# Kernel optimization log

Measured on AMD Instinct MI355X. Metric: run time of the kernel, lower is better.

The kernel has to match this reference:

```python
import jax, jax.numpy as jnp
import numpy as np
from jax import lax


def _box_conv3d(x, win):
    k = jnp.ones((1, 1, win, win, win), x.dtype) / float(win ** 3)
    pad = win // 2
    return lax.conv_general_dilated(
        x, k,
        window_strides=(1, 1, 1),
        padding=[(pad, pad)] * 3,
        dimension_numbers=('NCDHW', 'OIDHW', 'NCDHW'),
    )


def setup_inputs() -> dict:
    key = jax.random.key(0)
    k1, k2 = jax.random.split(key)
    shape = (1, 1, 160, 192, 224)
    pred = jax.random.uniform(k1, shape, dtype=jnp.float32)
    target = jax.random.uniform(k2, shape, dtype=jnp.float32)
    return {'pred': pred, 'target': target, 'window_size': 9}


def reference(pred, target, window_size):
    Ii = target
    Ji = pred
    win = window_size
    mu1 = _box_conv3d(Ii, win)
    mu2 = _box_conv3d(Ji, win)
    mu1_sq = mu1 * mu1
    mu2_sq = mu2 * mu2
    mu1_mu2 = mu1 * mu2
    sigma1_sq = _box_conv3d(Ii * Ii, win) - mu1_sq
    sigma2_sq = _box_conv3d(Ji * Ji, win) - mu2_sq
    sigma12 = _box_conv3d(Ii * Ji, win) - mu1_mu2
    eps = jnp.finfo(sigma12.dtype).eps
    cc = sigma12 * sigma12 / jnp.maximum(sigma1_sq * sigma2_sq, eps)
    return -jnp.mean(cc)
```

## Files before the change

kernel.cpp:

```cpp
#include <hip/hip_runtime.h>
#include <hip/hip_fp16.h>

#define D_  160
#define H_  192
#define W_  224
#define HW_ (H_ * W_)
#define HW2_ (HW_ / 2)
#define N_  (D_ * H_ * W_)
#define INV729 (1.0f / 729.0f)
#define HSEG 16
#define NSEG (H_ / HSEG)
#define NROW (HSEG + 9)
#define UPD  (NSEG * 2)


__device__ __forceinline__ unsigned pack2(float a, float b) {
    const __half2 h = __floats2half2_rn(a, b);
    return *(const unsigned*)&h;
}

__global__ __launch_bounds__(64) void k_passWH(const float* __restrict__ pred,
                                               const float* __restrict__ targ,
                                               uint4* __restrict__ outA,
                                               unsigned* __restrict__ outB,
                                               double* __restrict__ acc) {
    __shared__ __attribute__((aligned(16))) float2 lds[2][128];
    if (blockIdx.x == 0 && threadIdx.x == 0) *acc = 0.0;

    const int lane = threadIdx.x;
    const int unit = blockIdx.x;
    const int d    = unit / UPD;
    const int rem  = unit % UPD;
    const int half = rem & 1;
    const int h0   = (rem >> 1) * HSEG;
    const long dbase = (long)d * HW_;
    const int wbase = half * 112;

    const bool isld = (lane < 30);
    const int  w0c  = wbase - 4 + 4 * lane;
    const bool cok  = isld && (w0c >= 0) && (w0c + 3 < W_);
    const int  wsc  = w0c < 0 ? 0 : (w0c > W_ - 4 ? W_ - 4 : w0c);
    const float* gI = targ + dbase + wsc;
    const float* gJ = pred + dbase + wsc;

    float2 q[5][9];
    #pragma unroll
    for (int c = 0; c < 5; ++c)
        #pragma unroll
        for (int k = 0; k < 9; ++k) q[c][k] = make_float2(0.f, 0.f);
    float S0[5] = {0,0,0,0,0}, S1[5] = {0,0,0,0,0};

    float4 pI[3], pJ[3];
    auto fetch = [&](int r, float4& fi, float4& fj) {
        if (r >= NROW) { fi = make_float4(0.f,0.f,0.f,0.f); fj = fi; return; }
        const int hh = h0 - 5 + r;
        const int hc = hh < 0 ? 0 : (hh >= H_ ? H_ - 1 : hh);
        float4 a = *(const float4*)(gI + (long)hc * W_);
        float4 b = *(const float4*)(gJ + (long)hc * W_);
        if (!(cok && hh >= 0 && hh < H_)) {
            a = make_float4(0.f, 0.f, 0.f, 0.f); b = a;
        }
        fi = a; fj = b;
    };
    auto wr = [&](int row, int slot) {
        float2* dst = &lds[row & 1][4 * lane];
        *(float4*)(dst)     = make_float4(pI[slot].x, pJ[slot].x, pI[slot].y, pJ[slot].y);
        *(float4*)(dst + 2) = make_float4(pI[slot].z, pJ[slot].z, pI[slot].w, pJ[slot].w);
    };

    if (isld) {
        fetch(0, pI[0], pJ[0]);
        fetch(1, pI[1], pJ[1]);
        fetch(2, pI[2], pJ[2]);
        wr(0, 0);
        fetch(3, pI[0], pJ[0]);
    }

    #pragma unroll
    for (int p = 0; p < NROW; ++p) {
        if (isld) {
            wr(p + 1, (p + 1) % 3);
            fetch(p + 4, pI[(p + 1) % 3], pJ[(p + 1) % 3]);
        }

        if (lane < 56) {
            float x[10], y[10];
            #pragma unroll
            for (int m = 0; m < 5; ++m) {
                const float4 v = *(const float4*)&lds[p & 1][2 * lane + 2 * m];
                x[2*m] = v.x; y[2*m] = v.y; x[2*m+1] = v.z; y[2*m+1] = v.w;
            }
            float sI = 0.f, sJ = 0.f, sII = 0.f, sJJ = 0.f, sIJ = 0.f;
            #pragma unroll
            for (int kk = 0; kk < 9; ++kk) {
                sI  += x[kk];          sJ  += y[kk];
                sII = fmaf(x[kk], x[kk], sII);
                sJJ = fmaf(y[kk], y[kk], sJJ);
                sIJ = fmaf(x[kk], y[kk], sIJ);
            }
            float w0[5], w1[5];
            w0[0] = sI;  w1[0] = sI  + x[9] - x[0];
            w0[1] = sJ;  w1[1] = sJ  + y[9] - y[0];
            w0[2] = sII; w1[2] = sII + x[9]*x[9] - x[0]*x[0];
            w0[3] = sJJ; w1[3] = sJJ + y[9]*y[9] - y[0]*y[0];
            w0[4] = sIJ; w1[4] = sIJ + x[9]*y[9] - x[0]*y[0];

            const int ph = p % 9;
            #pragma unroll
            for (int c = 0; c < 5; ++c) {
                S0[c] += w0[c] - q[c][ph].x;
                S1[c] += w1[c] - q[c][ph].y;
                q[c][ph].x = w0[c];
                q[c][ph].y = w1[c];
            }
            if (p >= 9) {
                const long rb = dbase + (long)(h0 + p - 9) * W_;
                uint4 oA;
                oA.x = pack2(S0[0], S0[1]); oA.y = pack2(S0[2], S0[3]);
                oA.z = pack2(S1[0], S1[1]); oA.w = pack2(S1[2], S1[3]);
                outA[rb / 2 + half * 56 + lane] = oA;
                outB[rb / 2 + half * 56 + lane] = pack2(S0[4], S1[4]);
            }
        }
    }
}

__global__ __launch_bounds__(256) void k_passD(const uint4* __restrict__ bufA,
                                               const unsigned* __restrict__ bufB,
                                               double* __restrict__ acc) {
    const int DSEG = D_ / 8;
    const int p2 = blockIdx.x * blockDim.x + threadIdx.x;
    const int d0 = blockIdx.y * DSEG;

    float2 q[5][9], S[5];
    #pragma unroll
    for (int c = 0; c < 5; ++c) S[c] = make_float2(0.f, 0.f);

    #pragma unroll
    for (int k = 0; k < 9; ++k) {
        const int dd = d0 - 5 + k;
        uint4 va = make_uint4(0u, 0u, 0u, 0u);
        unsigned vb = 0u;
        if (dd >= 0) {
            va = bufA[(long)dd * HW2_ + p2];
            vb = bufB[(long)dd * HW2_ + p2];
        }
        const float2 a01 = __half22float2(*(const __half2*)&va.x);
        const float2 a23 = __half22float2(*(const __half2*)&va.y);
        const float2 b01 = __half22float2(*(const __half2*)&va.z);
        const float2 b23 = __half22float2(*(const __half2*)&va.w);
        const float2 c44 = __half22float2(*(const __half2*)&vb);
        q[0][k] = make_float2(a01.x, b01.x); S[0].x += a01.x; S[0].y += b01.x;
        q[1][k] = make_float2(a01.y, b01.y); S[1].x += a01.y; S[1].y += b01.y;
        q[2][k] = make_float2(a23.x, b23.x); S[2].x += a23.x; S[2].y += b23.x;
        q[3][k] = make_float2(a23.y, b23.y); S[3].x += a23.y; S[3].y += b23.y;
        q[4][k] = make_float2(c44.x, c44.y); S[4].x += c44.x; S[4].y += c44.y;
    }

    float myacc = 0.f;
    #pragma unroll
    for (int j = 0; j < DSEG; ++j) {
        const int dd = d0 + 4 + j;
        uint4 va = make_uint4(0u, 0u, 0u, 0u);
        unsigned vb = 0u;
        if (dd < D_) {
            va = bufA[(long)dd * HW2_ + p2];
            vb = bufB[(long)dd * HW2_ + p2];
        }
        const float2 a01 = __half22float2(*(const __half2*)&va.x);
        const float2 a23 = __half22float2(*(const __half2*)&va.y);
        const float2 b01 = __half22float2(*(const __half2*)&va.z);
        const float2 b23 = __half22float2(*(const __half2*)&va.w);
        const float2 c44 = __half22float2(*(const __half2*)&vb);
        const float2 nv[5] = {
            make_float2(a01.x, b01.x), make_float2(a01.y, b01.y),
            make_float2(a23.x, b23.x), make_float2(a23.y, b23.y),
            make_float2(c44.x, c44.y)
        };
        const int ph = j % 9;
        #pragma unroll
        for (int c = 0; c < 5; ++c) {
            S[c].x += nv[c].x - q[c][ph].x;
            S[c].y += nv[c].y - q[c][ph].y;
            q[c][ph] = nv[c];
        }
        #pragma unroll
        for (int e = 0; e < 2; ++e) {
            const float mu1 = (e ? S[0].y : S[0].x) * INV729;
            const float mu2 = (e ? S[1].y : S[1].x) * INV729;
            const float s1  = (e ? S[2].y : S[2].x) * INV729 - mu1 * mu1;
            const float s2  = (e ? S[3].y : S[3].x) * INV729 - mu2 * mu2;
            const float s12 = (e ? S[4].y : S[4].x) * INV729 - mu1 * mu2;
            const float den = fmaxf(s1 * s2, 1.1920929e-7f);
            myacc += (s12 * s12) / den;
        }
    }

    __shared__ float red[256];
    red[threadIdx.x] = myacc;
    __syncthreads();
    #pragma unroll
    for (int s = 128; s > 0; s >>= 1) {
        if (threadIdx.x < s) red[threadIdx.x] += red[threadIdx.x + s];
        __syncthreads();
    }
    if (threadIdx.x == 0) atomicAdd(acc, (double)red[0]);
}

__global__ void k_fin(const double* __restrict__ acc, float* __restrict__ out) {
    out[0] = (float)(-(*acc) / (double)N_);
}

extern "C" void kernel_launch(void* const* d_in, const int* in_sizes, int n_in,
                              void* d_out, int out_size, void* d_ws, size_t ws_size,
                              hipStream_t stream) {
    const float* pred = (const float*)d_in[0];
    const float* targ = (const float*)d_in[1];

    uint4*    bufA = (uint4*)d_ws;
    unsigned* bufB = (unsigned*)((char*)d_ws + (size_t)(N_ / 2) * 16);
    double*   acc  = (double*)((char*)d_ws + (size_t)(N_ / 2) * 16 + (size_t)(N_ / 2) * 4);
    float*    out  = (float*)d_out;

    k_passWH<<<D_ * UPD, 64, 0, stream>>>(pred, targ, bufA, bufB, acc);
    dim3 g3(HW2_ / 256, 8);
    k_passD<<<g3, 256, 0, stream>>>(bufA, bufB, acc);
    k_fin<<<1, 1, 0, stream>>>(acc, out);
}
```

Baseline: 58.37 us.

## Process two depth slices per WH block and store H-ring history as packed half

Each 64-lane block of the W/H box-sum pass now handles two depth slices (d and d+80), using 60 lanes for loads instead of 30 and running the per-row column-sum work twice. The launch grid is halved accordingly. To fit two slices' ring buffers in registers, the 9-entry H-direction history is stored as packed fp16 pairs, and the running sums subtract the rounded value that was actually stored. This raises load-lane utilisation and per-thread work, at the cost of more registers, fewer blocks, and extra half conversions.

```diff
diff --git a/kernel.cpp b/kernel.cpp
--- a/kernel.cpp
+++ b/kernel.cpp
@@ -24,31 +24,37 @@
                                                uint4* __restrict__ outA,
                                                unsigned* __restrict__ outB,
                                                double* __restrict__ acc) {
-    __shared__ __attribute__((aligned(16))) float2 lds[2][128];
+    __shared__ __attribute__((aligned(16))) float2 lds[2][2][128];
     if (blockIdx.x == 0 && threadIdx.x == 0) *acc = 0.0;
 
     const int lane = threadIdx.x;
     const int unit = blockIdx.x;
-    const int d    = unit / UPD;
+    const int dp   = unit / UPD;
     const int rem  = unit % UPD;
     const int half = rem & 1;
     const int h0   = (rem >> 1) * HSEG;
-    const long dbase = (long)d * HW_;
+    const long dbaseA = (long)dp * HW_;
+    const long dbaseB = (long)(dp + 80) * HW_;
     const int wbase = half * 112;
 
-    const bool isld = (lane < 30);
-    const int  w0c  = wbase - 4 + 4 * lane;
-    const bool cok  = isld && (w0c >= 0) && (w0c + 3 < W_);
+    const int  sj   = (lane < 30) ? lane : lane - 30;
+    const int  w0c  = wbase - 4 + 4 * sj;
+    const bool cokG = (lane < 60) && (w0c >= 0) && (w0c + 3 < W_);
     const int  wsc  = w0c < 0 ? 0 : (w0c > W_ - 4 ? W_ - 4 : w0c);
-    const float* gI = targ + dbase + wsc;
-    const float* gJ = pred + dbase + wsc;
-
-    float2 q[5][9];
-    #pragma unroll
-    for (int c = 0; c < 5; ++c)
+    const long sdb  = (lane < 30) ? dbaseA : dbaseB;
+    const int  sstr = (lane < 30) ? 0 : 1;
+    const float* gI = targ + sdb + wsc;
+    const float* gJ = pred + sdb + wsc;
+
+    unsigned q[2][5][9];
+    #pragma unroll
+    for (int s = 0; s < 2; ++s)
         #pragma unroll
-        for (int k = 0; k < 9; ++k) q[c][k] = make_float2(0.f, 0.f);
-    float S0[5] = {0,0,0,0,0}, S1[5] = {0,0,0,0,0};
+        for (int c = 0; c < 5; ++c)
+            #pragma unroll
+            for (int k = 0; k < 9; ++k) q[s][c][k] = 0u;
+    float S0[2][5] = {{0,0,0,0,0},{0,0,0,0,0}};
+    float S1[2][5] = {{0,0,0,0,0},{0,0,0,0,0}};
 
     float4 pI[3], pJ[3];
     auto fetch = [&](int r, float4& fi, float4& fj) {
@@ -57,18 +63,18 @@
         const int hc = hh < 0 ? 0 : (hh >= H_ ? H_ - 1 : hh);
         float4 a = *(const float4*)(gI + (long)hc * W_);
         float4 b = *(const float4*)(gJ + (long)hc * W_);
-        if (!(cok && hh >= 0 && hh < H_)) {
+        if (!(cokG && hh >= 0 && hh < H_)) {
             a = make_float4(0.f, 0.f, 0.f, 0.f); b = a;
         }
         fi = a; fj = b;
     };
     auto wr = [&](int row, int slot) {
-        float2* dst = &lds[row & 1][4 * lane];
+        float2* dst = &lds[sstr][row & 1][4 * sj];
         *(float4*)(dst)     = make_float4(pI[slot].x, pJ[slot].x, pI[slot].y, pJ[slot].y);
         *(float4*)(dst + 2) = make_float4(pI[slot].z, pJ[slot].z, pI[slot].w, pJ[slot].w);
     };
 
-    if (isld) {
+    if (lane < 60) {
         fetch(0, pI[0], pJ[0]);
         fetch(1, pI[1], pJ[1]);
         fetch(2, pI[2], pJ[2]);
@@ -78,48 +84,54 @@
 
     #pragma unroll
     for (int p = 0; p < NROW; ++p) {
-        if (isld) {
+        if (lane < 60) {
             wr(p + 1, (p + 1) % 3);
             fetch(p + 4, pI[(p + 1) % 3], pJ[(p + 1) % 3]);
         }
 
         if (lane < 56) {
-            float x[10], y[10];
-            #pragma unroll
-            for (int m = 0; m < 5; ++m) {
-                const float4 v = *(const float4*)&lds[p & 1][2 * lane + 2 * m];
-                x[2*m] = v.x; y[2*m] = v.y; x[2*m+1] = v.z; y[2*m+1] = v.w;
-            }
-            float sI = 0.f, sJ = 0.f, sII = 0.f, sJJ = 0.f, sIJ = 0.f;
-            #pragma unroll
-            for (int kk = 0; kk < 9; ++kk) {
-                sI  += x[kk];          sJ  += y[kk];
-                sII = fmaf(x[kk], x[kk], sII);
-                sJJ = fmaf(y[kk], y[kk], sJJ);
-                sIJ = fmaf(x[kk], y[kk], sIJ);
-            }
-            float w0[5], w1[5];
-            w0[0] = sI;  w1[0] = sI  + x[9] - x[0];
-            w0[1] = sJ;  w1[1] = sJ  + y[9] - y[0];
-            w0[2] = sII; w1[2] = sII + x[9]*x[9] - x[0]*x[0];
-            w0[3] = sJJ; w1[3] = sJJ + y[9]*y[9] - y[0]*y[0];
-            w0[4] = sIJ; w1[4] = sIJ + x[9]*y[9] - x[0]*y[0];
-
             const int ph = p % 9;
             #pragma unroll
-            for (int c = 0; c < 5; ++c) {
-                S0[c] += w0[c] - q[c][ph].x;
-                S1[c] += w1[c] - q[c][ph].y;
-                q[c][ph].x = w0[c];
-                q[c][ph].y = w1[c];
-            }
-            if (p >= 9) {
-                const long rb = dbase + (long)(h0 + p - 9) * W_;
-                uint4 oA;
-                oA.x = pack2(S0[0], S0[1]); oA.y = pack2(S0[2], S0[3]);
-                oA.z = pack2(S1[0], S1[1]); oA.w = pack2(S1[2], S1[3]);
-                outA[rb / 2 + half * 56 + lane] = oA;
-                outB[rb / 2 + half * 56 + lane] = pack2(S0[4], S1[4]);
+            for (int s = 0; s < 2; ++s) {
+                float x[10], y[10];
+                #pragma unroll
+                for (int m = 0; m < 5; ++m) {
+                    const float4 v = *(const float4*)&lds[s][p & 1][2 * lane + 2 * m];
+                    x[2*m] = v.x; y[2*m] = v.y; x[2*m+1] = v.z; y[2*m+1] = v.w;
+                }
+                float sI = 0.f, sJ = 0.f, sII = 0.f, sJJ = 0.f, sIJ = 0.f;
+                #pragma unroll
+                for (int kk = 0; kk < 9; ++kk) {
+                    sI  += x[kk];          sJ  += y[kk];
+                    sII = fmaf(x[kk], x[kk], sII);
+                    sJJ = fmaf(y[kk], y[kk], sJJ);
+                    sIJ = fmaf(x[kk], y[kk], sIJ);
+                }
+                float w0s[5], w1s[5];
+                w0s[0] = sI;  w1s[0] = sI  + x[9] - x[0];
+                w0s[1] = sJ;  w1s[1] = sJ  + y[9] - y[0];
+                w0s[2] = sII; w1s[2] = sII + x[9]*x[9] - x[0]*x[0];
+                w0s[3] = sJJ; w1s[3] = sJJ + y[9]*y[9] - y[0]*y[0];
+                w0s[4] = sIJ; w1s[4] = sIJ + x[9]*y[9] - x[0]*y[0];
+
+                #pragma unroll
+                for (int c = 0; c < 5; ++c) {
+                    const unsigned nq = pack2(w0s[c], w1s[c]);
+                    const float2 nf = __half22float2(*(const __half2*)&nq);
+                    const float2 of = __half22float2(*(const __half2*)&q[s][c][ph]);
+                    S0[s][c] += nf.x - of.x;
+                    S1[s][c] += nf.y - of.y;
+                    q[s][c][ph] = nq;
+                }
+                if (p >= 9) {
+                    const long db = s ? dbaseB : dbaseA;
+                    const long rb = db + (long)(h0 + p - 9) * W_;
+                    uint4 oA;
+                    oA.x = pack2(S0[s][0], S0[s][1]); oA.y = pack2(S0[s][2], S0[s][3]);
+                    oA.z = pack2(S1[s][0], S1[s][1]); oA.w = pack2(S1[s][2], S1[s][3]);
+                    outA[rb / 2 + half * 56 + lane] = oA;
+                    outB[rb / 2 + half * 56 + lane] = pack2(S0[s][4], S1[s][4]);
+                }
             }
         }
     }
@@ -222,7 +234,7 @@
     double*   acc  = (double*)((char*)d_ws + (size_t)(N_ / 2) * 16 + (size_t)(N_ / 2) * 4);
     float*    out  = (float*)d_out;
 
-    k_passWH<<<D_ * UPD, 64, 0, stream>>>(pred, targ, bufA, bufB, acc);
+    k_passWH<<<80 * UPD, 64, 0, stream>>>(pred, targ, bufA, bufB, acc);
     dim3 g3(HW2_ / 256, 8);
     k_passD<<<g3, 256, 0, stream>>>(bufA, bufB, acc);
     k_fin<<<1, 1, 0, stream>>>(acc, out);
```

New measurement: 55.73 us, median of 3. 1.05x faster.
